# Kernel optimization log

Measured on AMD Instinct MI355X. Metric: run time of the kernel, lower is better.

The kernel has to match this reference:

```python
import jax, jax.numpy as jnp
import numpy as np

CLASS_COUNT = 100
IN_FEATURES = 256
OUT_FEATURES = 256


def setup_inputs() -> dict:
    key = jax.random.key(0)
    k1, k2, k3, k4 = jax.random.split(key, 4)
    N, C, H, W = 32, IN_FEATURES, 64, 64
    x = jax.random.normal(k1, (N, C, H, W), dtype=jnp.float32)
    classes = jax.random.randint(k2, (N,), 0, CLASS_COUNT, dtype=jnp.int32)
    # kaiming_uniform_(a=sqrt(5)) on [class_count, out, in]: fan_in = in_features
    fan_in = IN_FEATURES
    gain = np.sqrt(2.0 / (1.0 + 5.0))  # leaky_relu gain with a=sqrt(5)
    wbound = gain * np.sqrt(3.0 / fan_in)
    weight = jax.random.uniform(k3, (CLASS_COUNT, OUT_FEATURES, IN_FEATURES),
                                dtype=jnp.float32, minval=-wbound, maxval=wbound)
    bbound = 1.0 / np.sqrt(fan_in)
    bias = jax.random.uniform(k4, (CLASS_COUNT, OUT_FEATURES),
                              dtype=jnp.float32, minval=-bbound, maxval=bbound)
    return {"x": x, "classes": classes, "weight": weight, "bias": bias}


def reference(x, classes, weight, bias):
    # Per-sample weight/bias gather then 1x1 conv == batched matmul over pixels.
    w = weight[classes]          # [N, O, C]
    b = bias[classes]            # [N, O]
    out = jnp.einsum('nchw,noc->nohw', x, w)
    return out + b[:, :, None, None]
```

## Files before the change

### kernel.cpp

```cpp
#include <hip/hip_runtime.h>

#define CIN    256
#define COUT   256
#define PTOT   4096
#define BM     128
#define BN     128
#define BK     32
#define KSTEPS 8
#define LDSK   48

typedef __attribute__((ext_vector_type(8)))  short bfrag;
typedef __attribute__((ext_vector_type(16))) float f32x16;

__device__ __forceinline__ unsigned int f2bf(float f) {
    unsigned int x = __float_as_uint(f);
    x += 0x7fffu + ((x >> 16) & 1u);
    return x >> 16;
}

__device__ __forceinline__ int swz(int row, int k) {
    return k ^ (((row >> 2) & 3) << 3);
}

__device__ __forceinline__ f32x16 zero16() {
    f32x16 v;
    #pragma unroll
    for (int i = 0; i < 16; ++i) v[i] = 0.0f;
    return v;
}

__global__ __launch_bounds__(256, 3)
void selconv_mfma(const float* __restrict__ x,
                  const int*   __restrict__ classes,
                  const float* __restrict__ weight,
                  const float* __restrict__ bias,
                  float*       __restrict__ out)
{
    __shared__ unsigned short As[2][BM * LDSK];
    __shared__ unsigned short Bs[2][BN * LDSK];
    __shared__ float bias_s[BM];

    const int b     = blockIdx.x;
    const int xcd   = b & 7;
    const int local = b >> 3;
    const int n     = xcd * 4 + (local >> 6);
    const int rem   = local & 63;
    const int o0    = (rem >> 5) * BM;
    const int p0    = (rem & 31) * BN;

    const int tid  = threadIdx.x;
    const int lane = tid & 63;
    const int wid  = tid >> 6;
    const int wr   = wid >> 1;
    const int wc   = wid & 1;

    const int cls = classes[n];
    const float* Wn = weight + (size_t)cls * (COUT * CIN) + (size_t)o0 * CIN;
    const float* Xn = x   + (size_t)n * (CIN * PTOT) + p0;
    float*       On = out + (size_t)n * (COUT * PTOT) + (size_t)o0 * PTOT + p0;

    if (tid < BM) bias_s[tid] = bias[cls * COUT + o0 + tid];

    const int a_row0 = tid >> 3;
    const int a_col  = (tid & 7) * 4;
    const int b_p4   = (tid & 31) * 4;
    const int b_kp   = (tid >> 5) * 2;

    float4 A0[4], A1[4];
    float4 B0[4], B1[4];

    auto loadA = [&](float4 (&A)[4], int t) {
        const int k0 = t * BK;
        #pragma unroll
        for (int i = 0; i < 4; ++i)
            A[i] = *(const float4*)(Wn + (size_t)(a_row0 + 32 * i) * CIN + k0 + a_col);
    };
    auto loadB = [&](float4 (&B)[4], int t) {
        const int k0 = t * BK;
        #pragma unroll
        for (int j = 0; j < 2; ++j) {
            const int kr = k0 + b_kp + 16 * j;
            B[j * 2 + 0] = *(const float4*)(Xn + (size_t)kr       * PTOT + b_p4);
            B[j * 2 + 1] = *(const float4*)(Xn + (size_t)(kr + 1) * PTOT + b_p4);
        }
    };
    auto writeT = [&](int buf, float4 (&A)[4], float4 (&B)[4]) {
        #pragma unroll
        for (int i = 0; i < 4; ++i) {
            const int row = a_row0 + 32 * i;
            uint2 w;
            w.x = f2bf(A[i].x) | (f2bf(A[i].y) << 16);
            w.y = f2bf(A[i].z) | (f2bf(A[i].w) << 16);
            *(uint2*)(&As[buf][row * LDSK + swz(row, a_col)]) = w;
        }
        #pragma unroll
        for (int j = 0; j < 2; ++j) {
            const int kk = b_kp + 16 * j;
            const float pa[4] = {B[j*2+0].x, B[j*2+0].y, B[j*2+0].z, B[j*2+0].w};
            const float pb[4] = {B[j*2+1].x, B[j*2+1].y, B[j*2+1].z, B[j*2+1].w};
            #pragma unroll
            for (int i = 0; i < 4; ++i) {
                const int p = b_p4 + i;
                const unsigned int w = f2bf(pa[i]) | (f2bf(pb[i]) << 16);
                *(unsigned int*)(&Bs[buf][p * LDSK + swz(p, kk)]) = w;
            }
        }
    };

    const int fr  = lane & 31;
    const int fg8 = (lane >> 5) * 8;
    f32x16 acc00 = zero16(), acc01 = zero16(), acc10 = zero16(), acc11 = zero16();

    auto mfma_step = [&](int buf) {
        const unsigned short* Ab = As[buf];
        const unsigned short* Bb = Bs[buf];
        const int rowA0 = wr * 64 + fr;
        const int colB0 = wc * 64 + fr;
        #pragma unroll
        for (int s = 0; s < 2; ++s) {
            const int kof = s * 16 + fg8;
            bfrag a0 = *(const bfrag*)(&Ab[(rowA0     ) * LDSK + swz(rowA0,      kof)]);
            bfrag a1 = *(const bfrag*)(&Ab[(rowA0 + 32) * LDSK + swz(rowA0 + 32, kof)]);
            bfrag b0 = *(const bfrag*)(&Bb[(colB0     ) * LDSK + swz(colB0,      kof)]);
            bfrag b1 = *(const bfrag*)(&Bb[(colB0 + 32) * LDSK + swz(colB0 + 32, kof)]);
            acc00 = __builtin_amdgcn_mfma_f32_32x32x16_bf16(a0, b0, acc00, 0, 0, 0);
            acc01 = __builtin_amdgcn_mfma_f32_32x32x16_bf16(a0, b1, acc01, 0, 0, 0);
            acc10 = __builtin_amdgcn_mfma_f32_32x32x16_bf16(a1, b0, acc10, 0, 0, 0);
            acc11 = __builtin_amdgcn_mfma_f32_32x32x16_bf16(a1, b1, acc11, 0, 0, 0);
        }
    };

    loadA(A0, 0); loadB(B0, 0);
    loadA(A1, 1); loadB(B1, 1);
    writeT(0, A0, B0);
    __syncthreads();

    #pragma unroll
    for (int t = 0; t < KSTEPS; t += 2) {
        if (t + 2 < KSTEPS) { loadA(A0, t + 2); loadB(B0, t + 2); }
        mfma_step(0);
        writeT(1, A1, B1);
        __syncthreads();
        if (t + 3 < KSTEPS) { loadA(A1, t + 3); loadB(B1, t + 3); }
        mfma_step(1);
        if (t + 2 < KSTEPS) { writeT(0, A0, B0); __syncthreads(); }
    }

    const int col = lane & 31;
    const int rh  = (lane >> 5) * 4;

    auto store_frag = [&](f32x16 a, int mi, int nj) {
        const int ob = wr * 64 + mi * 32;
        const int pc = wc * 64 + nj * 32 + col;
        #pragma unroll
        for (int r = 0; r < 16; ++r) {
            const int row = (r & 3) + 8 * (r >> 2) + rh;
            const int o   = ob + row;
            On[(size_t)o * PTOT + pc] = a[r] + bias_s[o];
        }
    };
    store_frag(acc00, 0, 0);
    store_frag(acc01, 0, 1);
    store_frag(acc10, 1, 0);
    store_frag(acc11, 1, 1);
}

extern "C" void kernel_launch(void* const* d_in, const int* in_sizes, int n_in,
                              void* d_out, int out_size, void* d_ws, size_t ws_size,
                              hipStream_t stream) {
    const float* x       = (const float*)d_in[0];
    const int*   classes = (const int*)d_in[1];
    const float* weight  = (const float*)d_in[2];
    const float* bias    = (const float*)d_in[3];
    float*       out     = (float*)d_out;

    const int grid = 32 * (COUT / BM) * (PTOT / BN);
    selconv_mfma<<<grid, 256, 0, stream>>>(x, classes, weight, bias, out);
}
```

Baseline: 62.83 us.

## Store X tile as k-pair-packed rows in LDS and pad A without swizzle

The B (activation) tile is now stored in LDS as packed bf16 k-pairs in a [k/2][p] layout. Each thread writes one 16-byte vector instead of eight scalar 4-byte writes, and fragment reads become four 32-bit LDS loads per operand instead of one 16-byte load. The A tile drops the XOR swizzle in favour of a padded row stride of 40, which also shrinks LDS use, and launch bounds are raised to target 4 blocks per CU. The aim is cheaper LDS stores and higher occupancy, at the cost of more LDS read instructions in the inner MFMA loop and possible bank conflicts on the padded A reads.

```diff
diff --git a/kernel.cpp b/kernel.cpp
--- a/kernel.cpp
+++ b/kernel.cpp
@@ -7,19 +7,17 @@
 #define BN     128
 #define BK     32
 #define KSTEPS 8
-#define LDSK   48
+#define LDSA   40
 
 typedef __attribute__((ext_vector_type(8)))  short bfrag;
 typedef __attribute__((ext_vector_type(16))) float f32x16;
+
+union U4F { uint4 u; bfrag f; };
 
 __device__ __forceinline__ unsigned int f2bf(float f) {
     unsigned int x = __float_as_uint(f);
     x += 0x7fffu + ((x >> 16) & 1u);
     return x >> 16;
-}
-
-__device__ __forceinline__ int swz(int row, int k) {
-    return k ^ (((row >> 2) & 3) << 3);
 }
 
 __device__ __forceinline__ f32x16 zero16() {
@@ -29,15 +27,15 @@
     return v;
 }
 
-__global__ __launch_bounds__(256, 3)
+__global__ __launch_bounds__(256, 4)
 void selconv_mfma(const float* __restrict__ x,
                   const int*   __restrict__ classes,
                   const float* __restrict__ weight,
                   const float* __restrict__ bias,
                   float*       __restrict__ out)
 {
-    __shared__ unsigned short As[2][BM * LDSK];
-    __shared__ unsigned short Bs[2][BN * LDSK];
+    __shared__ __align__(16) unsigned short As[2][BM * LDSA];
+    __shared__ __align__(16) unsigned int   Bs[2][(BK / 2) * BN];
     __shared__ float bias_s[BM];
 
     const int b     = blockIdx.x;
@@ -63,8 +61,8 @@
 
     const int a_row0 = tid >> 3;
     const int a_col  = (tid & 7) * 4;
+    const int b_kp   = tid >> 5;
     const int b_p4   = (tid & 31) * 4;
-    const int b_kp   = (tid >> 5) * 2;
 
     float4 A0[4], A1[4];
     float4 B0[4], B1[4];
@@ -79,7 +77,7 @@
         const int k0 = t * BK;
         #pragma unroll
         for (int j = 0; j < 2; ++j) {
-            const int kr = k0 + b_kp + 16 * j;
+            const int kr = k0 + 2 * (b_kp + 8 * j);
             B[j * 2 + 0] = *(const float4*)(Xn + (size_t)kr       * PTOT + b_p4);
             B[j * 2 + 1] = *(const float4*)(Xn + (size_t)(kr + 1) * PTOT + b_p4);
         }
@@ -91,19 +89,19 @@
             uint2 w;
             w.x = f2bf(A[i].x) | (f2bf(A[i].y) << 16);
             w.y = f2bf(A[i].z) | (f2bf(A[i].w) << 16);
-            *(uint2*)(&As[buf][row * LDSK + swz(row, a_col)]) = w;
+            *(uint2*)(&As[buf][row * LDSA + a_col]) = w;
         }
         #pragma unroll
         for (int j = 0; j < 2; ++j) {
-            const int kk = b_kp + 16 * j;
-            const float pa[4] = {B[j*2+0].x, B[j*2+0].y, B[j*2+0].z, B[j*2+0].w};
-            const float pb[4] = {B[j*2+1].x, B[j*2+1].y, B[j*2+1].z, B[j*2+1].w};
-            #pragma unroll
-            for (int i = 0; i < 4; ++i) {
-                const int p = b_p4 + i;
-                const unsigned int w = f2bf(pa[i]) | (f2bf(pb[i]) << 16);
-                *(unsigned int*)(&Bs[buf][p * LDSK + swz(p, kk)]) = w;
-            }
+            const int kp = b_kp + 8 * j;
+            const float4 e = B[j * 2 + 0];
+            const float4 o = B[j * 2 + 1];
+            uint4 w;
+            w.x = f2bf(e.x) | (f2bf(o.x) << 16);
+            w.y = f2bf(e.y) | (f2bf(o.y) << 16);
+            w.z = f2bf(e.z) | (f2bf(o.z) << 16);
+            w.w = f2bf(e.w) | (f2bf(o.w) << 16);
+            *(uint4*)(&Bs[buf][kp * BN + b_p4]) = w;
         }
     };
 
@@ -113,20 +111,28 @@
 
     auto mfma_step = [&](int buf) {
         const unsigned short* Ab = As[buf];
-        const unsigned short* Bb = Bs[buf];
+        const unsigned int*   Bb = Bs[buf];
         const int rowA0 = wr * 64 + fr;
-        const int colB0 = wc * 64 + fr;
+        const int pB0   = wc * 64 + fr;
         #pragma unroll
         for (int s = 0; s < 2; ++s) {
             const int kof = s * 16 + fg8;
-            bfrag a0 = *(const bfrag*)(&Ab[(rowA0     ) * LDSK + swz(rowA0,      kof)]);
-            bfrag a1 = *(const bfrag*)(&Ab[(rowA0 + 32) * LDSK + swz(rowA0 + 32, kof)]);
-            bfrag b0 = *(const bfrag*)(&Bb[(colB0     ) * LDSK + swz(colB0,      kof)]);
-            bfrag b1 = *(const bfrag*)(&Bb[(colB0 + 32) * LDSK + swz(colB0 + 32, kof)]);
-            acc00 = __builtin_amdgcn_mfma_f32_32x32x16_bf16(a0, b0, acc00, 0, 0, 0);
-            acc01 = __builtin_amdgcn_mfma_f32_32x32x16_bf16(a0, b1, acc01, 0, 0, 0);
-            acc10 = __builtin_amdgcn_mfma_f32_32x32x16_bf16(a1, b0, acc10, 0, 0, 0);
-            acc11 = __builtin_amdgcn_mfma_f32_32x32x16_bf16(a1, b1, acc11, 0, 0, 0);
+            const int kp0 = kof >> 1;
+            bfrag a0 = *(const bfrag*)(&Ab[(rowA0     ) * LDSA + kof]);
+            bfrag a1 = *(const bfrag*)(&Ab[(rowA0 + 32) * LDSA + kof]);
+            U4F ub0, ub1;
+            ub0.u.x = Bb[(kp0 + 0) * BN + pB0];
+            ub0.u.y = Bb[(kp0 + 1) * BN + pB0];
+            ub0.u.z = Bb[(kp0 + 2) * BN + pB0];
+            ub0.u.w = Bb[(kp0 + 3) * BN + pB0];
+            ub1.u.x = Bb[(kp0 + 0) * BN + pB0 + 32];
+            ub1.u.y = Bb[(kp0 + 1) * BN + pB0 + 32];
+            ub1.u.z = Bb[(kp0 + 2) * BN + pB0 + 32];
+            ub1.u.w = Bb[(kp0 + 3) * BN + pB0 + 32];
+            acc00 = __builtin_amdgcn_mfma_f32_32x32x16_bf16(a0, ub0.f, acc00, 0, 0, 0);
+            acc01 = __builtin_amdgcn_mfma_f32_32x32x16_bf16(a0, ub1.f, acc01, 0, 0, 0);
+            acc10 = __builtin_amdgcn_mfma_f32_32x32x16_bf16(a1, ub0.f, acc10, 0, 0, 0);
+            acc11 = __builtin_amdgcn_mfma_f32_32x32x16_bf16(a1, ub1.f, acc11, 0, 0, 0);
         }
     };
 
```

Measured after the change: 224.9 us. 258% more time.
